# Optimization experiments

Measured on AMD Instinct MI355X. Metric: run time of the kernel, lower is better.

The kernel has to match this reference:

```python
import jax, jax.numpy as jnp
import numpy as np

N = 50000
E = 800000
DIN = 128
DH = [128, 128]
DOUT = 64


def setup_inputs() -> dict:
    key = jax.random.key(0)
    ks = jax.random.split(key, 12)

    def w(k, fan_in, fan_out):
        return jax.random.normal(k, (fan_in, fan_out), dtype=jnp.float32) / np.sqrt(fan_in)

    x = jax.random.normal(ks[0], (N, DIN), dtype=jnp.float32)
    edge_index = jax.random.randint(ks[1], (2, E), 0, N, dtype=jnp.int64)
    return {
        "x": x,
        "edge_index": edge_index,
        # SAGEConv layer 0: lin_l (aggregated neighbors, with bias), lin_r (root, no bias)
        "Wl0": w(ks[2], DIN, DH[0]), "Wr0": w(ks[3], DIN, DH[0]), "b0": jnp.zeros((DH[0],), jnp.float32),
        # SAGEConv layer 1
        "Wl1": w(ks[4], DH[0], DH[1]), "Wr1": w(ks[5], DH[0], DH[1]), "b1": jnp.zeros((DH[1],), jnp.float32),
        # final Linear
        "Wout": w(ks[6], DH[1], DOUT), "bout": jnp.zeros((DOUT,), jnp.float32),
    }


def sage_conv(h, src, dst, Wl, Wr, b):
    # mean-aggregate source features at destination nodes
    msg = h[src]                                                  # [E, d]
    agg = jax.ops.segment_sum(msg, dst, num_segments=N)           # [N, d]
    cnt = jax.ops.segment_sum(jnp.ones((src.shape[0],), h.dtype), dst, num_segments=N)
    agg = agg / jnp.maximum(cnt, 1.0)[:, None]
    return agg @ Wl + h @ Wr + b


def reference(x, edge_index, Wl0, Wr0, b0, Wl1, Wr1, b1, Wout, bout):
    src, dst = edge_index[0], edge_index[1]
    h = jax.nn.relu(sage_conv(x, src, dst, Wl0, Wr0, b0))
    # dropout: identity in eval mode
    h = jax.nn.relu(sage_conv(h, src, dst, Wl1, Wr1, b1))
    out = h @ Wout + bout                                         # [N, DOUT]
    return jax.nn.softmax(out, axis=1)
```

## Files before the change

### kernel.cpp

```cpp
#include <hip/hip_runtime.h>


#define CAP 64
#define NBK 256
#define EPB 2048
#define ASTR 136

typedef __attribute__((ext_vector_type(8))) short bf16x8;
typedef __attribute__((ext_vector_type(4))) float f32x4;

__device__ __forceinline__ unsigned short bf16_rtne(float f) {
    unsigned u = __float_as_uint(f);
    u += 0x7FFFu + ((u >> 16) & 1u);
    return (unsigned short)(u >> 16);
}

__device__ __forceinline__ unsigned pack2(float lo, float hi) {
    return (unsigned)bf16_rtne(lo) | ((unsigned)bf16_rtne(hi) << 16);
}

__device__ __forceinline__ void pack_w_body(const float* __restrict__ Wl,
                                            const float* __restrict__ Wr,
                                            unsigned short* __restrict__ Wp, int i) {
    int j = i & 7;
    int l = (i >> 3) & 63;
    int ntile = (i >> 9) & 7;
    int kstep = i >> 12;
    int k = kstep * 32 + (l >> 4) * 8 + j;
    int n = ntile * 16 + (l & 15);
    float v = (k < 128) ? Wl[k * 128 + n] : Wr[(k - 128) * 128 + n];
    Wp[i] = bf16_rtne(v);
}

__global__ __launch_bounds__(256) void bucket_prep_kernel(
        const int* __restrict__ src, const int* __restrict__ dst,
        unsigned int* __restrict__ pref2, unsigned int* __restrict__ gbuf,
        int E, int aBlocks,
        const float* __restrict__ x, unsigned short* __restrict__ xb, int n4, int cvtBlocks,
        const float* __restrict__ Wl0, const float* __restrict__ Wr0,
        unsigned short* __restrict__ Wp1,
        const float* __restrict__ Wl1, const float* __restrict__ Wr1,
        unsigned short* __restrict__ Wp2,
        const float* __restrict__ Wout, unsigned short* __restrict__ Wpo) {
    int b = blockIdx.x;
    if (b < aBlocks) {
        __shared__ unsigned int hist[NBK];
        __shared__ unsigned int pref[NBK + 1];
        __shared__ unsigned int scat[EPB];
        int tid = (int)threadIdx.x;
        hist[tid] = 0u;
        __syncthreads();

        int e0 = b * EPB + tid * 8;
        int dd[8], ss[8], bb[8];
        unsigned rr[8];
        bool vld[8];
        if (e0 + 7 < E) {
            int4 d0 = *(const int4*)(dst + e0);
            int4 d1 = *(const int4*)(dst + e0 + 4);
            int4 s0 = *(const int4*)(src + e0);
            int4 s1 = *(const int4*)(src + e0 + 4);
            dd[0] = d0.x; dd[1] = d0.y; dd[2] = d0.z; dd[3] = d0.w;
            dd[4] = d1.x; dd[5] = d1.y; dd[6] = d1.z; dd[7] = d1.w;
            ss[0] = s0.x; ss[1] = s0.y; ss[2] = s0.z; ss[3] = s0.w;
            ss[4] = s1.x; ss[5] = s1.y; ss[6] = s1.z; ss[7] = s1.w;
#pragma unroll
            for (int u = 0; u < 8; ++u) vld[u] = true;
        } else {
#pragma unroll
            for (int u = 0; u < 8; ++u) {
                int e = e0 + u;
                vld[u] = (e < E);
                dd[u] = vld[u] ? dst[e] : 0;
                ss[u] = vld[u] ? src[e] : 0;
            }
        }
#pragma unroll
        for (int u = 0; u < 8; ++u) {
            bb[u] = dd[u] >> 8;
            rr[u] = vld[u] ? atomicAdd(&hist[bb[u]], 1u) : 0u;
        }
        __syncthreads();
        pref[tid + 1] = hist[tid];
        if (tid == 0) pref[0] = 0u;
        __syncthreads();
        for (int off = 1; off < NBK; off <<= 1) {
            unsigned add = (tid + 1 > off) ? pref[tid + 1 - off] : 0u;
            __syncthreads();
            pref[tid + 1] += add;
            __syncthreads();
        }
#pragma unroll
        for (int u = 0; u < 8; ++u) {
            if (vld[u]) {
                unsigned idx = pref[bb[u]] + rr[u];
                scat[idx] = ((unsigned)dd[u] << 16) | (unsigned)(ss[u] & 0xFFFF);
            }
        }
        __syncthreads();
        {
            uint4* g4 = (uint4*)(gbuf + (size_t)b * EPB);
            const uint4* s4 = (const uint4*)scat;
            for (int i = tid; i < EPB / 4; i += 256) g4[i] = s4[i];
        }
        pref2[(size_t)b * NBK + tid] = (pref[tid] & 0xFFFFu) | (pref[tid + 1] << 16);
    } else if (b < aBlocks + cvtBlocks) {
        int i = (b - aBlocks) * 256 + (int)threadIdx.x;
        if (i < n4) {
            float4 v = ((const float4*)x)[i];
            ushort4 o;
            o.x = bf16_rtne(v.x); o.y = bf16_rtne(v.y);
            o.z = bf16_rtne(v.z); o.w = bf16_rtne(v.w);
            ((ushort4*)xb)[i] = o;
        }
    } else if (b < aBlocks + cvtBlocks + 128) {
        pack_w_body(Wl0, Wr0, Wp1, (b - aBlocks - cvtBlocks) * 256 + (int)threadIdx.x);
    } else if (b < aBlocks + cvtBlocks + 256) {
        pack_w_body(Wl1, Wr1, Wp2, (b - aBlocks - cvtBlocks - 128) * 256 + (int)threadIdx.x);
    } else {
        int i = (b - aBlocks - cvtBlocks - 256) * 256 + (int)threadIdx.x;
        int j = i & 7;
        int l = (i >> 3) & 63;
        int nt = (i >> 9) & 3;
        int ks = i >> 11;
        int k = ks * 32 + (l >> 4) * 8 + j;
        int n = nt * 16 + (l & 15);
        Wpo[i] = bf16_rtne(Wout[k * 64 + n]);
    }
}

__global__ __launch_bounds__(256) void fill_csr_kernel(
        const unsigned int* __restrict__ pref2, const unsigned int* __restrict__ gbuf,
        int* __restrict__ cnt, unsigned short* __restrict__ csr, int N, int aBlocks) {
    __shared__ unsigned int cntL[256];
    __shared__ unsigned short stage[256 * CAP];
    int bk = blockIdx.x;
    int tid = (int)threadIdx.x;
    cntL[tid] = 0u;
    __syncthreads();
    for (int b = tid; b < aBlocks; b += 256) {
        unsigned pr = pref2[(size_t)b * NBK + bk];
        unsigned st = pr & 0xFFFFu;
        unsigned en = pr >> 16;
        const unsigned int* slab = gbuf + (size_t)b * EPB;
        for (unsigned i = st; i < en; ++i) {
            unsigned pk = slab[i];
            int dl = (int)((pk >> 16) & 255u);
            unsigned p = atomicAdd(&cntL[dl], 1u);
            if (p < CAP) stage[dl * CAP + p] = (unsigned short)(pk & 0xFFFFu);
        }
    }
    __syncthreads();
    const uint4* s4 = (const uint4*)stage;
    uint4* g4 = (uint4*)(csr + (size_t)bk * (256 * CAP));
    for (int i = tid; i < (256 * CAP) / 8; i += 256) g4[i] = s4[i];
    int node = bk * 256 + tid;
    if (node < N) cnt[node] = min((int)cntL[tid], CAP);
}

__device__ __forceinline__ void gather_mean_lds(
        const uint4* __restrict__ h4,
        const int* __restrict__ cnt,
        const unsigned short* __restrict__ csr, unsigned short* __restrict__ sAw,
        int m0, int lane, int N) {
    int qw = lane >> 4;
    int ql = lane & 15;
#pragma unroll 1
    for (int i = 0; i < 4; ++i) {
        int nl = qw * 4 + i;
        int node = m0 + nl;
        int deg = (node < N) ? min(cnt[node], CAP) : 0;
        int s0 = node * CAP;
        int s1 = s0 + deg;
        float a[8];
#pragma unroll
        for (int u = 0; u < 8; ++u) a[u] = 0.f;
        for (int base = 0; base < deg; base += 16) {
            int nc = min(16, deg - base);
            int e = min(s0 + base + ql, s1 - 1);
            int idx = csr[e];
            for (int j = 0; j < nc; j += 8) {
                uint4 v[8];
#pragma unroll
                for (int u = 0; u < 8; ++u) {
                    int sidx = __shfl(idx, j + u, 16);
                    v[u] = h4[(size_t)sidx * 16 + ql];
                }
#pragma unroll
                for (int u = 0; u < 8; ++u) {
                    bool ok = (j + u < nc);
                    unsigned w0 = ok ? v[u].x : 0u;
                    unsigned w1 = ok ? v[u].y : 0u;
                    unsigned w2 = ok ? v[u].z : 0u;
                    unsigned w3 = ok ? v[u].w : 0u;
                    a[0] += __uint_as_float(w0 << 16);
                    a[1] += __uint_as_float(w0 & 0xFFFF0000u);
                    a[2] += __uint_as_float(w1 << 16);
                    a[3] += __uint_as_float(w1 & 0xFFFF0000u);
                    a[4] += __uint_as_float(w2 << 16);
                    a[5] += __uint_as_float(w2 & 0xFFFF0000u);
                    a[6] += __uint_as_float(w3 << 16);
                    a[7] += __uint_as_float(w3 & 0xFFFF0000u);
                }
            }
        }
        float inv = 1.0f / (float)max(deg, 1);
        uint4 o;
        o.x = pack2(a[0] * inv, a[1] * inv);
        o.y = pack2(a[2] * inv, a[3] * inv);
        o.z = pack2(a[4] * inv, a[5] * inv);
        o.w = pack2(a[6] * inv, a[7] * inv);
        *(uint4*)(sAw + nl * ASTR + ql * 8) = o;
    }
}

__device__ __forceinline__ void mfma_dual_gemm_lds(
        const unsigned short* __restrict__ sAw, const unsigned short* __restrict__ rootb,
        const unsigned short* __restrict__ Wp, int rowc, int quad, int c, int lane,
        f32x4 acc[8]) {
#pragma unroll
    for (int t = 0; t < 8; ++t) acc[t] = (f32x4){0.f, 0.f, 0.f, 0.f};
    for (int ks = 0; ks < 8; ++ks) {
        bf16x8 a;
        if (ks < 4) a = *(const bf16x8*)(sAw + c * ASTR + ks * 32 + quad * 8);
        else        a = *(const bf16x8*)(rootb + (size_t)rowc * 128 + (ks & 3) * 32 + quad * 8);
#pragma unroll
        for (int t = 0; t < 8; ++t) {
            bf16x8 bf = *(const bf16x8*)(Wp + ((size_t)(ks * 8 + t) * 64 + lane) * 8);
            acc[t] = __builtin_amdgcn_mfma_f32_16x16x32_bf16(a, bf, acc[t], 0, 0, 0);
        }
    }
}

__global__ __launch_bounds__(256) void fused_l1_kernel(
        const unsigned short* __restrict__ hb, const int* __restrict__ cnt,
        const unsigned short* __restrict__ csr, const unsigned short* __restrict__ Wp,
        const float* __restrict__ b, unsigned short* __restrict__ houtb, int N) {
    __shared__ unsigned short sA[4][16 * ASTR];
    int lane = threadIdx.x & 63;
    int wv = threadIdx.x >> 6;
    int m0 = blockIdx.x * 64 + wv * 16;
    gather_mean_lds((const uint4*)hb, cnt, csr, &sA[wv][0], m0, lane, N);
    int quad = lane >> 4;
    int c = lane & 15;
    int rowc = min(m0 + c, N - 1);
    f32x4 acc[8];
    mfma_dual_gemm_lds(&sA[wv][0], hb, Wp, rowc, quad, c, lane, acc);
#pragma unroll
    for (int t = 0; t < 8; ++t) {
        int col = t * 16 + c;
        float bias = b[col];
#pragma unroll
        for (int r = 0; r < 4; ++r) {
            sA[wv][(quad * 4 + r) * ASTR + col] = bf16_rtne(fmaxf(acc[t][r] + bias, 0.f));
        }
    }
    {
        int qw = lane >> 4, ql = lane & 15;
#pragma unroll
        for (int i = 0; i < 4; ++i) {
            int nl = qw * 4 + i;
            int node = m0 + nl;
            if (node < N) {
                uint4 row = *(const uint4*)(&sA[wv][nl * ASTR + ql * 8]);
                *(uint4*)(houtb + (size_t)node * 128 + ql * 8) = row;
            }
        }
    }
}

__global__ __launch_bounds__(256) void fused_l2_kernel(
        const unsigned short* __restrict__ hb, const int* __restrict__ cnt,
        const unsigned short* __restrict__ csr, const unsigned short* __restrict__ Wp,
        const float* __restrict__ b,
        const unsigned short* __restrict__ Wpo, const float* __restrict__ bout,
        float* __restrict__ out, int N) {
    __shared__ unsigned short sA[4][16 * ASTR];
    int lane = threadIdx.x & 63;
    int wv = threadIdx.x >> 6;
    int m0 = blockIdx.x * 64 + wv * 16;
    gather_mean_lds((const uint4*)hb, cnt, csr, &sA[wv][0], m0, lane, N);
    int quad = lane >> 4;
    int c = lane & 15;
    int rowc = min(m0 + c, N - 1);
    f32x4 acc[8];
    mfma_dual_gemm_lds(&sA[wv][0], hb, Wp, rowc, quad, c, lane, acc);
#pragma unroll
    for (int t = 0; t < 8; ++t) {
        int col = t * 16 + c;
        float bias = b[col];
#pragma unroll
        for (int r = 0; r < 4; ++r) {
            sA[wv][(quad * 4 + r) * ASTR + col] = bf16_rtne(fmaxf(acc[t][r] + bias, 0.f));
        }
    }

    f32x4 acc2[4];
#pragma unroll
    for (int nt = 0; nt < 4; ++nt) acc2[nt] = (f32x4){0.f, 0.f, 0.f, 0.f};
#pragma unroll
    for (int ks = 0; ks < 4; ++ks) {
        bf16x8 a = *(const bf16x8*)&sA[wv][c * ASTR + ks * 32 + quad * 8];
#pragma unroll
        for (int nt = 0; nt < 4; ++nt) {
            bf16x8 bf = *(const bf16x8*)(Wpo + ((size_t)(ks * 4 + nt) * 64 + lane) * 8);
            acc2[nt] = __builtin_amdgcn_mfma_f32_16x16x32_bf16(a, bf, acc2[nt], 0, 0, 0);
        }
    }

    float bo[4];
#pragma unroll
    for (int nt = 0; nt < 4; ++nt) bo[nt] = bout[nt * 16 + c];
#pragma unroll
    for (int r = 0; r < 4; ++r) {
        float v[4];
#pragma unroll
        for (int nt = 0; nt < 4; ++nt) v[nt] = acc2[nt][r] + bo[nt];
        float m = fmaxf(fmaxf(v[0], v[1]), fmaxf(v[2], v[3]));
#pragma unroll
        for (int ofs = 1; ofs < 16; ofs <<= 1) m = fmaxf(m, __shfl_xor(m, ofs, 64));
        float e[4];
        float s = 0.f;
#pragma unroll
        for (int nt = 0; nt < 4; ++nt) { e[nt] = __expf(v[nt] - m); s += e[nt]; }
#pragma unroll
        for (int ofs = 1; ofs < 16; ofs <<= 1) s += __shfl_xor(s, ofs, 64);
        float inv = 1.0f / s;
        int node = m0 + quad * 4 + r;
        if (node < N) {
#pragma unroll
            for (int nt = 0; nt < 4; ++nt)
                out[(size_t)node * 64 + nt * 16 + c] = e[nt] * inv;
        }
    }
}

extern "C" void kernel_launch(void* const* d_in, const int* in_sizes, int n_in,
                              void* d_out, int out_size, void* d_ws, size_t ws_size,
                              hipStream_t stream) {
    const float* x    = (const float*)d_in[0];
    const int*   ei   = (const int*)d_in[1];
    const float* Wl0  = (const float*)d_in[2];
    const float* Wr0  = (const float*)d_in[3];
    const float* b0   = (const float*)d_in[4];
    const float* Wl1  = (const float*)d_in[5];
    const float* Wr1  = (const float*)d_in[6];
    const float* b1   = (const float*)d_in[7];
    const float* Wout = (const float*)d_in[8];
    const float* bout = (const float*)d_in[9];

    int N = in_sizes[0] / 128;
    int E = in_sizes[1] / 2;
    const int* src = ei;
    const int* dst = ei + E;
    int nb = (N + 255) >> 8;
    int aBlocks = (E + EPB - 1) / EPB;

    char* p = (char*)d_ws;
    auto alloc = [&](size_t bytes) -> char* {
        char* r = p;
        p += (bytes + 255) & ~(size_t)255;
        return r;
    };
    unsigned int*   pref2 = (unsigned int*)alloc((size_t)aBlocks * NBK * 4);
    unsigned int*   gbuf  = (unsigned int*)alloc((size_t)aBlocks * EPB * 4);
    int*            cnt   = (int*)alloc((size_t)N * 4);
    unsigned short* csr   = (unsigned short*)alloc((size_t)nb * 256 * CAP * 2);
    unsigned short* xb    = (unsigned short*)alloc((size_t)N * 128 * 2);
    unsigned short* h0b   = (unsigned short*)alloc((size_t)N * 128 * 2);
    unsigned short* Wp1   = (unsigned short*)alloc((size_t)32768 * 2);
    unsigned short* Wp2   = (unsigned short*)alloc((size_t)32768 * 2);
    unsigned short* Wpo   = (unsigned short*)alloc((size_t)8192 * 2);

    int n4 = N * 128 / 4;
    int cvtBlocks = (n4 + 255) / 256;
    bucket_prep_kernel<<<aBlocks + cvtBlocks + 256 + 32, 256, 0, stream>>>(
        src, dst, pref2, gbuf, E, aBlocks,
        x, xb, n4, cvtBlocks, Wl0, Wr0, Wp1, Wl1, Wr1, Wp2, Wout, Wpo);

    fill_csr_kernel<<<nb, 256, 0, stream>>>(pref2, gbuf, cnt, csr, N, aBlocks);

    int gb = (N + 63) / 64;
    fused_l1_kernel<<<gb, 256, 0, stream>>>(xb, cnt, csr, Wp1, b0, h0b, N);
    fused_l2_kernel<<<gb, 256, 0, stream>>>(h0b, cnt, csr, Wp2, b1,
                                            Wpo, bout, (float*)d_out, N);
}
```

Baseline: 187.1 us.

## Split each 16-node tile across two waves sharing gather and GEMM columns

Blocks shrink from four independent waves (64 nodes) to two cooperating waves handling 16 nodes. Each wave gathers half the rows into a shared LDS tile, then computes half of the output columns of the dual GEMM. This halves per-wave accumulator registers and the weight traffic per wave, and spreads the grid over more blocks. In exchange it adds block-level barriers and leaves one wave idle during the final projection and softmax in layer 2.

```diff
diff --git a/kernel.cpp b/kernel.cpp
--- a/kernel.cpp
+++ b/kernel.cpp
@@ -158,16 +158,16 @@
     if (node < N) cnt[node] = min((int)cntL[tid], CAP);
 }
 
-__device__ __forceinline__ void gather_mean_lds(
+__device__ __forceinline__ void gather_mean_lds2(
         const uint4* __restrict__ h4,
         const int* __restrict__ cnt,
         const unsigned short* __restrict__ csr, unsigned short* __restrict__ sAw,
-        int m0, int lane, int N) {
+        int m0, int wv, int lane, int N) {
     int qw = lane >> 4;
     int ql = lane & 15;
 #pragma unroll 1
-    for (int i = 0; i < 4; ++i) {
-        int nl = qw * 4 + i;
+    for (int i = 0; i < 2; ++i) {
+        int nl = wv * 8 + qw * 2 + i;
         int node = m0 + nl;
         int deg = (node < N) ? min(cnt[node], CAP) : 0;
         int s0 = node * CAP;
@@ -214,93 +214,102 @@
     }
 }
 
-__device__ __forceinline__ void mfma_dual_gemm_lds(
+__device__ __forceinline__ void mfma_dual_gemm_half(
         const unsigned short* __restrict__ sAw, const unsigned short* __restrict__ rootb,
         const unsigned short* __restrict__ Wp, int rowc, int quad, int c, int lane,
-        f32x4 acc[8]) {
-#pragma unroll
-    for (int t = 0; t < 8; ++t) acc[t] = (f32x4){0.f, 0.f, 0.f, 0.f};
+        int wv, f32x4 acc[4]) {
+#pragma unroll
+    for (int t = 0; t < 4; ++t) acc[t] = (f32x4){0.f, 0.f, 0.f, 0.f};
     for (int ks = 0; ks < 8; ++ks) {
         bf16x8 a;
         if (ks < 4) a = *(const bf16x8*)(sAw + c * ASTR + ks * 32 + quad * 8);
         else        a = *(const bf16x8*)(rootb + (size_t)rowc * 128 + (ks & 3) * 32 + quad * 8);
 #pragma unroll
-        for (int t = 0; t < 8; ++t) {
-            bf16x8 bf = *(const bf16x8*)(Wp + ((size_t)(ks * 8 + t) * 64 + lane) * 8);
+        for (int t = 0; t < 4; ++t) {
+            int tt = wv * 4 + t;
+            bf16x8 bf = *(const bf16x8*)(Wp + ((size_t)(ks * 8 + tt) * 64 + lane) * 8);
             acc[t] = __builtin_amdgcn_mfma_f32_16x16x32_bf16(a, bf, acc[t], 0, 0, 0);
         }
     }
 }
 
-__global__ __launch_bounds__(256) void fused_l1_kernel(
+__global__ __launch_bounds__(128) void fused_l1_kernel(
         const unsigned short* __restrict__ hb, const int* __restrict__ cnt,
         const unsigned short* __restrict__ csr, const unsigned short* __restrict__ Wp,
         const float* __restrict__ b, unsigned short* __restrict__ houtb, int N) {
-    __shared__ unsigned short sA[4][16 * ASTR];
-    int lane = threadIdx.x & 63;
-    int wv = threadIdx.x >> 6;
-    int m0 = blockIdx.x * 64 + wv * 16;
-    gather_mean_lds((const uint4*)hb, cnt, csr, &sA[wv][0], m0, lane, N);
+    __shared__ unsigned short sA[16 * ASTR];
+    int tid = (int)threadIdx.x;
+    int lane = tid & 63;
+    int wv = tid >> 6;
+    int m0 = blockIdx.x * 16;
+    gather_mean_lds2((const uint4*)hb, cnt, csr, sA, m0, wv, lane, N);
+    __syncthreads();
     int quad = lane >> 4;
     int c = lane & 15;
     int rowc = min(m0 + c, N - 1);
-    f32x4 acc[8];
-    mfma_dual_gemm_lds(&sA[wv][0], hb, Wp, rowc, quad, c, lane, acc);
-#pragma unroll
-    for (int t = 0; t < 8; ++t) {
-        int col = t * 16 + c;
+    f32x4 acc[4];
+    mfma_dual_gemm_half(sA, hb, Wp, rowc, quad, c, lane, wv, acc);
+    __syncthreads();
+#pragma unroll
+    for (int t = 0; t < 4; ++t) {
+        int col = (wv * 4 + t) * 16 + c;
         float bias = b[col];
 #pragma unroll
         for (int r = 0; r < 4; ++r) {
-            sA[wv][(quad * 4 + r) * ASTR + col] = bf16_rtne(fmaxf(acc[t][r] + bias, 0.f));
-        }
-    }
-    {
-        int qw = lane >> 4, ql = lane & 15;
-#pragma unroll
-        for (int i = 0; i < 4; ++i) {
-            int nl = qw * 4 + i;
-            int node = m0 + nl;
-            if (node < N) {
-                uint4 row = *(const uint4*)(&sA[wv][nl * ASTR + ql * 8]);
-                *(uint4*)(houtb + (size_t)node * 128 + ql * 8) = row;
-            }
-        }
-    }
-}
-
-__global__ __launch_bounds__(256) void fused_l2_kernel(
+            sA[(quad * 4 + r) * ASTR + col] = bf16_rtne(fmaxf(acc[t][r] + bias, 0.f));
+        }
+    }
+    __syncthreads();
+#pragma unroll
+    for (int it = 0; it < 2; ++it) {
+        int chunk = it * 128 + tid;
+        int row = chunk >> 4;
+        int ql = chunk & 15;
+        int node = m0 + row;
+        if (node < N) {
+            uint4 rv = *(const uint4*)(&sA[row * ASTR + ql * 8]);
+            *(uint4*)(houtb + (size_t)node * 128 + ql * 8) = rv;
+        }
+    }
+}
+
+__global__ __launch_bounds__(128) void fused_l2_kernel(
         const unsigned short* __restrict__ hb, const int* __restrict__ cnt,
         const unsigned short* __restrict__ csr, const unsigned short* __restrict__ Wp,
         const float* __restrict__ b,
         const unsigned short* __restrict__ Wpo, const float* __restrict__ bout,
         float* __restrict__ out, int N) {
-    __shared__ unsigned short sA[4][16 * ASTR];
-    int lane = threadIdx.x & 63;
-    int wv = threadIdx.x >> 6;
-    int m0 = blockIdx.x * 64 + wv * 16;
-    gather_mean_lds((const uint4*)hb, cnt, csr, &sA[wv][0], m0, lane, N);
+    __shared__ unsigned short sA[16 * ASTR];
+    int tid = (int)threadIdx.x;
+    int lane = tid & 63;
+    int wv = tid >> 6;
+    int m0 = blockIdx.x * 16;
+    gather_mean_lds2((const uint4*)hb, cnt, csr, sA, m0, wv, lane, N);
+    __syncthreads();
     int quad = lane >> 4;
     int c = lane & 15;
     int rowc = min(m0 + c, N - 1);
-    f32x4 acc[8];
-    mfma_dual_gemm_lds(&sA[wv][0], hb, Wp, rowc, quad, c, lane, acc);
-#pragma unroll
-    for (int t = 0; t < 8; ++t) {
-        int col = t * 16 + c;
+    f32x4 acc[4];
+    mfma_dual_gemm_half(sA, hb, Wp, rowc, quad, c, lane, wv, acc);
+    __syncthreads();
+#pragma unroll
+    for (int t = 0; t < 4; ++t) {
+        int col = (wv * 4 + t) * 16 + c;
         float bias = b[col];
 #pragma unroll
         for (int r = 0; r < 4; ++r) {
-            sA[wv][(quad * 4 + r) * ASTR + col] = bf16_rtne(fmaxf(acc[t][r] + bias, 0.f));
-        }
-    }
+            sA[(quad * 4 + r) * ASTR + col] = bf16_rtne(fmaxf(acc[t][r] + bias, 0.f));
+        }
+    }
+    __syncthreads();
+    if (wv != 0) return;
 
     f32x4 acc2[4];
 #pragma unroll
     for (int nt = 0; nt < 4; ++nt) acc2[nt] = (f32x4){0.f, 0.f, 0.f, 0.f};
 #pragma unroll
     for (int ks = 0; ks < 4; ++ks) {
-        bf16x8 a = *(const bf16x8*)&sA[wv][c * ASTR + ks * 32 + quad * 8];
+        bf16x8 a = *(const bf16x8*)&sA[c * ASTR + ks * 32 + quad * 8];
 #pragma unroll
         for (int nt = 0; nt < 4; ++nt) {
             bf16x8 bf = *(const bf16x8*)(Wpo + ((size_t)(ks * 4 + nt) * 64 + lane) * 8);
@@ -380,8 +389,8 @@
 
     fill_csr_kernel<<<nb, 256, 0, stream>>>(pref2, gbuf, cnt, csr, N, aBlocks);
 
-    int gb = (N + 63) / 64;
-    fused_l1_kernel<<<gb, 256, 0, stream>>>(xb, cnt, csr, Wp1, b0, h0b, N);
-    fused_l2_kernel<<<gb, 256, 0, stream>>>(h0b, cnt, csr, Wp2, b1,
+    int gb = (N + 15) / 16;
+    fused_l1_kernel<<<gb, 128, 0, stream>>>(xb, cnt, csr, Wp1, b0, h0b, N);
+    fused_l2_kernel<<<gb, 128, 0, stream>>>(h0b, cnt, csr, Wp2, b1,
                                             Wpo, bout, (float*)d_out, N);
 }
```

Result: no change. 184.1 us (-1.6%).
